# Optimization experiments

Hardware: AMD Instinct MI355X
Metric: run time of the kernel (lower is better)

## Reference

```python
import jax, jax.numpy as jnp
import numpy as np

B, L, C, D = 32, 256, 16, 128
WORD_VOCAB, CHR_VOCAB = 50000, 128


def conv1d(x, w, b):
    # x: [N, D, T], w: [D_out, D_in, 3], torch Conv1d (cross-correlation), padding=1
    y = jax.lax.conv_general_dilated(x, w, window_strides=(1,), padding=[(1, 1)],
                                     dimension_numbers=('NCH', 'OIH', 'NCH'))
    return y + b[None, :, None]


def setup_inputs() -> dict:
    key = jax.random.key(0)
    k1, k2, k3, k4, k5, k6, k7, k8 = jax.random.split(key, 8)
    word_vector = jax.random.randint(k1, (B, L), 0, WORD_VOCAB)
    words_in_char = jax.random.randint(k2, (B, L, C), 0, CHR_VOCAB)
    # embedding tables, padding_idx=0 -> row 0 is zeros
    word_table = (jax.random.normal(k3, (WORD_VOCAB, D), jnp.float32) * 0.02).at[0].set(0.0)
    chr_table = (jax.random.normal(k4, (CHR_VOCAB, D), jnp.float32) * 0.02).at[0].set(0.0)
    scale = 1.0 / np.sqrt(D * 3)
    conv_chr_w = jax.random.normal(k5, (D, D, 3), jnp.float32) * scale
    conv_chr_b = jax.random.normal(k6, (D,), jnp.float32) * scale
    conv_word_w = jax.random.normal(k7, (D, D, 3), jnp.float32) * scale
    conv_word_b = jax.random.normal(k8, (D,), jnp.float32) * scale
    return dict(word_vector=word_vector, words_in_char=words_in_char,
                word_table=word_table, chr_table=chr_table,
                conv_chr_w=conv_chr_w, conv_chr_b=conv_chr_b,
                conv_word_w=conv_word_w, conv_word_b=conv_word_b)


def reference(word_vector, words_in_char, word_table, chr_table,
              conv_chr_w, conv_chr_b, conv_word_w, conv_word_b):
    # --- char path (batched version of the per-word Python loop) ---
    chr_emb = chr_table[words_in_char]                       # [B, L, C, D]
    x = chr_emb.reshape(B * L, C, D).transpose(0, 2, 1)      # [B*L, D, C]
    word_conv = conv1d(x, conv_chr_w, conv_chr_b)            # [B*L, D, C]
    char_feats = word_conv.max(axis=2).reshape(B, L, D)      # max over char positions
    # --- word path ---
    word_emb = word_table[word_vector]                       # [B, L, D]
    out = conv1d(word_emb.transpose(0, 2, 1), conv_word_w, conv_word_b)  # [B, D, L]
    # stack both branch outputs into one array: [2, B, D, L]
    return jnp.stack([out, char_feats.transpose(0, 2, 1)])
```

## Files before the change

kernel.cpp:

```cpp
#include <hip/hip_runtime.h>

typedef __attribute__((ext_vector_type(8))) short short8;
typedef __attribute__((ext_vector_type(2))) float float2_t;
typedef __attribute__((ext_vector_type(4))) float float4_t;
typedef __attribute__((ext_vector_type(16))) float float16_t;

#define NB 32
#define NL 256
#define ND 128
#define OUT_PLANE (NB * ND * NL)
#define XS 136
#define BUFSZ (18 * XS)
#define FR_WORD 49152
#define CHRB 98304

__device__ inline unsigned short f2bf(float f) {
    union { float f; unsigned int i; } c;
    c.f = f;
    unsigned int r = c.i + 0x7FFFu + ((c.i >> 16) & 1u);
    return (unsigned short)(r >> 16);
}

__global__ void make_frags(const float* __restrict__ Wc,
                           const float* __restrict__ Ww,
                           const float* __restrict__ chrT,
                           unsigned short* __restrict__ out) {
    int i = blockIdx.x * 256 + threadIdx.x;
    if (i < FR_WORD) {
        int j    = i & 7;
        int lane = (i >> 3) & 63;
        int nt   = (i >> 9) & 3;
        int s    = i >> 11;
        int dout = nt * 32 + (lane & 31);
        int kk   = s * 16 + ((lane >> 5) & 1) * 8 + j;
        int t    = kk >> 7;
        int d    = kk & 127;
        out[i] = f2bf(Wc[(dout * 128 + d) * 3 + t]);
    } else if (i < CHRB) {
        int ii = i - FR_WORD;
        int j    = ii & 7;
        int lane = (ii >> 3) & 63;
        int nt   = (ii >> 9) & 7;
        int s    = ii >> 12;
        int dout = nt * 16 + (lane & 15);
        int t    = s >> 2;
        int k    = (s & 3) * 32 + ((lane >> 4) & 3) * 8 + j;
        out[i] = f2bf(Ww[(dout * 128 + k) * 3 + t]);
    } else {
        int j = i - CHRB;
        out[i] = f2bf(chrT[j]);
    }
}

__global__ __launch_bounds__(128, 2) void conv_kernel(
    const int* __restrict__ wv, const int* __restrict__ wic,
    const float* __restrict__ wordT,
    const unsigned short* __restrict__ ws,
    const float* __restrict__ biasC, const float* __restrict__ biasW,
    float* __restrict__ out) {
    __shared__ unsigned short X[4][BUFSZ];
    const int tid  = threadIdx.x;
    const int wave = tid >> 6, lane = tid & 63;
    const int bid = blockIdx.x;

    if (bid >= 512) {
        const unsigned short* chrB = ws + CHRB;
        const int w0 = (bid - 512) * 8;
        const int b = w0 >> 8, l0 = w0 & 255;
        const int n32 = lane & 31;
        const int h   = (lane >> 5) & 1;
        const int r15 = lane & 15;
        const int wsel = (lane >> 4) & 1;

        short8 bfrag[24][2];
#pragma unroll
        for (int s = 0; s < 24; ++s)
#pragma unroll
            for (int p = 0; p < 2; ++p)
                bfrag[s][p] = *(const short8*)(
                    ws + (((s * 4 + wave * 2 + p) * 64 + lane) << 3));

        for (int p = tid; p < XS; p += 128)
#pragma unroll
            for (int q = 0; q < 4; ++q) { X[q][p] = 0; X[q][17 * XS + p] = 0; }

        const int ra = tid >> 4, sub = tid & 15;

#pragma unroll
        for (int q = 0; q < 2; ++q) {
            int j0 = wic[(w0 + q) * 16 + ra];
            int j1 = wic[(w0 + q) * 16 + ra + 8];
            short8 g0 = *(const short8*)(chrB + j0 * 128 + sub * 8);
            short8 g1 = *(const short8*)(chrB + j1 * 128 + sub * 8);
            *(short8*)&X[q][(ra + 1) * XS + sub * 8] = g0;
            *(short8*)&X[q][(ra + 9) * XS + sub * 8] = g1;
        }
        int iA0 = wic[(w0 + 2) * 16 + ra];
        int iA1 = wic[(w0 + 2) * 16 + ra + 8];
        int iC0 = wic[(w0 + 3) * 16 + ra];
        int iC1 = wic[(w0 + 3) * 16 + ra + 8];
        __syncthreads();

#pragma unroll
        for (int j = 0; j < 8; j += 2) {
            const unsigned short* abuf = X[(j + wsel) & 3];

            short8 g0, g1;
            if (j < 6) {
                g0 = *(const short8*)(chrB + iA0 * 128 + sub * 8);
                g1 = *(const short8*)(chrB + iA1 * 128 + sub * 8);
            }

            float16_t acc[2];
#pragma unroll
            for (int p = 0; p < 2; ++p)
#pragma unroll
                for (int e = 0; e < 16; ++e) acc[p][e] = 0.f;

#pragma unroll
            for (int s = 0; s < 12; ++s) {
                short8 a = *(const short8*)&abuf[(r15 + (s >> 3)) * XS +
                                                 (s & 7) * 16 + h * 8];
#pragma unroll
                for (int p = 0; p < 2; ++p)
                    acc[p] = __builtin_amdgcn_mfma_f32_32x32x16_bf16(
                        a, bfrag[s][p], acc[p], 0, 0, 0);
            }

            short8 h0, h1;
            if (j < 6) {
                *(short8*)&X[(j + 2) & 3][(ra + 1) * XS + sub * 8] = g0;
                *(short8*)&X[(j + 2) & 3][(ra + 9) * XS + sub * 8] = g1;
                h0 = *(const short8*)(chrB + iC0 * 128 + sub * 8);
                h1 = *(const short8*)(chrB + iC1 * 128 + sub * 8);
                if (j < 4) {
                    iA0 = wic[(w0 + j + 4) * 16 + ra];
                    iA1 = wic[(w0 + j + 4) * 16 + ra + 8];
                    iC0 = wic[(w0 + j + 5) * 16 + ra];
                    iC1 = wic[(w0 + j + 5) * 16 + ra + 8];
                }
            }

#pragma unroll
            for (int s = 12; s < 24; ++s) {
                short8 a = *(const short8*)&abuf[(r15 + (s >> 3)) * XS +
                                                 (s & 7) * 16 + h * 8];
#pragma unroll
                for (int p = 0; p < 2; ++p)
                    acc[p] = __builtin_amdgcn_mfma_f32_32x32x16_bf16(
                        a, bfrag[s][p], acc[p], 0, 0, 0);
            }

            if (j < 6) {
                *(short8*)&X[(j + 3) & 3][(ra + 1) * XS + sub * 8] = h0;
                *(short8*)&X[(j + 3) & 3][(ra + 9) * XS + sub * 8] = h1;
            }

#pragma unroll
            for (int p = 0; p < 2; ++p) {
                float v0 = acc[p][0], v1 = acc[p][8];
#pragma unroll
                for (int e = 1; e < 8; ++e) {
                    v0 = fmaxf(v0, acc[p][e]);
                    v1 = fmaxf(v1, acc[p][e + 8]);
                }
                v0 = fmaxf(v0, __shfl_xor(v0, 32, 64));
                v1 = fmaxf(v1, __shfl_xor(v1, 32, 64));
                int dout = wave * 64 + p * 32 + n32;
                if (lane < 32) {
                    float bc = biasC[dout];
                    float2_t st = {v0 + bc, v1 + bc};
                    *(float2_t*)&out[OUT_PLANE + b * (ND * NL) + dout * NL +
                                     l0 + j] = st;
                }
            }
            __syncthreads();
        }
    } else {
        const int m = lane & 15, quad = lane >> 4;
        const int b = bid >> 4, l0 = (bid & 15) << 4;
        short8 bfrag[12][4];
#pragma unroll
        for (int s = 0; s < 12; ++s)
#pragma unroll
            for (int p = 0; p < 4; ++p)
                bfrag[s][p] = *(const short8*)(
                    ws + FR_WORD + (((s * 8 + wave * 4 + p) * 64 + lane) << 3));
        float bb[4];
#pragma unroll
        for (int p = 0; p < 4; ++p) bb[p] = biasW[wave * 64 + p * 16 + m];

#pragma unroll
        for (int i0 = 0; i0 < 2; ++i0) {
            int i = tid + i0 * 128;
            if (i < 144) {
                int rr = i >> 3, sg = i & 7;
                int l = l0 + rr - 1;
                int idx = (l >= 0 && l < NL) ? wv[b * NL + l] : 0;
                const float4_t* src =
                    (const float4_t*)(wordT + idx * 128 + sg * 16);
                float4_t f0 = src[0], f1 = src[1], f2 = src[2], f3 = src[3];
                unsigned short t16[16];
                t16[0]=f2bf(f0.x); t16[1]=f2bf(f0.y); t16[2]=f2bf(f0.z); t16[3]=f2bf(f0.w);
                t16[4]=f2bf(f1.x); t16[5]=f2bf(f1.y); t16[6]=f2bf(f1.z); t16[7]=f2bf(f1.w);
                t16[8]=f2bf(f2.x); t16[9]=f2bf(f2.y); t16[10]=f2bf(f2.z); t16[11]=f2bf(f2.w);
                t16[12]=f2bf(f3.x); t16[13]=f2bf(f3.y); t16[14]=f2bf(f3.z); t16[15]=f2bf(f3.w);
                *(short8*)&X[0][rr * XS + sg * 16]     = *(const short8*)&t16[0];
                *(short8*)&X[0][rr * XS + sg * 16 + 8] = *(const short8*)&t16[8];
            }
        }
        __syncthreads();

        float4_t acc[4];
#pragma unroll
        for (int p = 0; p < 4; ++p) acc[p] = (float4_t){0.f, 0.f, 0.f, 0.f};
#pragma unroll
        for (int s = 0; s < 12; ++s) {
            short8 a = *(const short8*)&X[0][(m + (s >> 2)) * XS +
                                            (s & 3) * 32 + quad * 8];
#pragma unroll
            for (int p = 0; p < 4; ++p)
                acc[p] = __builtin_amdgcn_mfma_f32_16x16x32_bf16(
                    a, bfrag[s][p], acc[p], 0, 0, 0);
        }

        float* obase = out + b * (ND * NL) + l0 + quad * 4;
#pragma unroll
        for (int p = 0; p < 4; ++p) {
            int dout = wave * 64 + p * 16 + m;
            float4_t pk;
            pk.x = acc[p].x + bb[p];
            pk.y = acc[p].y + bb[p];
            pk.z = acc[p].z + bb[p];
            pk.w = acc[p].w + bb[p];
            *(float4_t*)&obase[dout * NL] = pk;
        }
    }
}

extern "C" void kernel_launch(void* const* d_in, const int* in_sizes, int n_in,
                              void* d_out, int out_size, void* d_ws,
                              size_t ws_size, hipStream_t stream) {
    const int* word_vector   = (const int*)d_in[0];
    const int* words_in_char = (const int*)d_in[1];
    const float* word_table  = (const float*)d_in[2];
    const float* chr_table   = (const float*)d_in[3];
    const float* conv_chr_w  = (const float*)d_in[4];
    const float* conv_chr_b  = (const float*)d_in[5];
    const float* conv_word_w = (const float*)d_in[6];
    const float* conv_word_b = (const float*)d_in[7];
    float* out            = (float*)d_out;
    unsigned short* wsp   = (unsigned short*)d_ws;

    make_frags<<<448, 256, 0, stream>>>(conv_chr_w, conv_word_w, chr_table, wsp);
    conv_kernel<<<1536, 128, 0, stream>>>(word_vector, words_in_char,
                                          word_table, wsp,
                                          conv_chr_b, conv_word_b, out);
}
```

Before: 105.4 us.

## Fuse fragment prep into conv kernel with grid-wide atomic barrier

Merges the bf16 weight/table conversion kernel into the main conv kernel. Each block converts a slice of the workspace, then all blocks wait on a global atomic counter before continuing. The grid shrinks from 1536 to 1024 blocks: every block does a char-path tile, and the first 512 also do a word-path tile. This drops one kernel launch and the gap between launches, but adds a hipMemsetAsync and a spin barrier. The barrier relies on all 1024 blocks being resident at once and can deadlock if they are not.

```diff
diff --git a/kernel.cpp b/kernel.cpp
--- a/kernel.cpp
+++ b/kernel.cpp
@@ -13,6 +13,9 @@
 #define BUFSZ (18 * XS)
 #define FR_WORD 49152
 #define CHRB 98304
+#define WS_ELEMS 114688
+#define FLAG_BYTE_OFF (WS_ELEMS * 2)
+#define GRID 1024
 
 __device__ inline unsigned short f2bf(float f) {
     union { float f; unsigned int i; } c;
@@ -21,51 +24,63 @@
     return (unsigned short)(r >> 16);
 }
 
-__global__ void make_frags(const float* __restrict__ Wc,
-                           const float* __restrict__ Ww,
-                           const float* __restrict__ chrT,
-                           unsigned short* __restrict__ out) {
-    int i = blockIdx.x * 256 + threadIdx.x;
-    if (i < FR_WORD) {
-        int j    = i & 7;
-        int lane = (i >> 3) & 63;
-        int nt   = (i >> 9) & 3;
-        int s    = i >> 11;
-        int dout = nt * 32 + (lane & 31);
-        int kk   = s * 16 + ((lane >> 5) & 1) * 8 + j;
-        int t    = kk >> 7;
-        int d    = kk & 127;
-        out[i] = f2bf(Wc[(dout * 128 + d) * 3 + t]);
-    } else if (i < CHRB) {
-        int ii = i - FR_WORD;
-        int j    = ii & 7;
-        int lane = (ii >> 3) & 63;
-        int nt   = (ii >> 9) & 7;
-        int s    = ii >> 12;
-        int dout = nt * 16 + (lane & 15);
-        int t    = s >> 2;
-        int k    = (s & 3) * 32 + ((lane >> 4) & 3) * 8 + j;
-        out[i] = f2bf(Ww[(dout * 128 + k) * 3 + t]);
-    } else {
-        int j = i - CHRB;
-        out[i] = f2bf(chrT[j]);
-    }
-}
-
-__global__ __launch_bounds__(128, 2) void conv_kernel(
+__global__ __launch_bounds__(128, 2) void conv_all(
     const int* __restrict__ wv, const int* __restrict__ wic,
-    const float* __restrict__ wordT,
-    const unsigned short* __restrict__ ws,
+    const float* __restrict__ wordT, const float* __restrict__ chrT,
+    const float* __restrict__ Wc, const float* __restrict__ Ww,
     const float* __restrict__ biasC, const float* __restrict__ biasW,
+    unsigned short* __restrict__ wsp, unsigned int* __restrict__ flag,
     float* __restrict__ out) {
     __shared__ unsigned short X[4][BUFSZ];
     const int tid  = threadIdx.x;
     const int wave = tid >> 6, lane = tid & 63;
     const int bid = blockIdx.x;
 
-    if (bid >= 512) {
-        const unsigned short* chrB = ws + CHRB;
-        const int w0 = (bid - 512) * 8;
+    if (tid < 112) {
+        int i = bid * 112 + tid;
+        unsigned short val;
+        if (i < FR_WORD) {
+            int j    = i & 7;
+            int ln   = (i >> 3) & 63;
+            int nt   = (i >> 9) & 3;
+            int s    = i >> 11;
+            int dout = nt * 32 + (ln & 31);
+            int kk   = s * 16 + ((ln >> 5) & 1) * 8 + j;
+            int t    = kk >> 7;
+            int d    = kk & 127;
+            val = f2bf(Wc[(dout * 128 + d) * 3 + t]);
+        } else if (i < CHRB) {
+            int ii = i - FR_WORD;
+            int j    = ii & 7;
+            int ln   = (ii >> 3) & 63;
+            int nt   = (ii >> 9) & 7;
+            int s    = ii >> 12;
+            int dout = nt * 16 + (ln & 15);
+            int t    = s >> 2;
+            int k    = (s & 3) * 32 + ((ln >> 4) & 3) * 8 + j;
+            val = f2bf(Ww[(dout * 128 + k) * 3 + t]);
+        } else {
+            val = f2bf(chrT[i - CHRB]);
+        }
+        wsp[i] = val;
+    }
+    for (int p = tid; p < XS; p += 128)
+#pragma unroll
+        for (int q = 0; q < 4; ++q) { X[q][p] = 0; X[q][17 * XS + p] = 0; }
+
+    __threadfence();
+    __syncthreads();
+    if (tid == 0) {
+        atomicAdd(flag, 1u);
+        while (*(volatile unsigned int*)flag < (unsigned int)GRID)
+            __builtin_amdgcn_s_sleep(8);
+    }
+    __syncthreads();
+    __threadfence();
+
+    {
+        const unsigned short* chrB = wsp + CHRB;
+        const int w0 = bid * 8;
         const int b = w0 >> 8, l0 = w0 & 255;
         const int n32 = lane & 31;
         const int h   = (lane >> 5) & 1;
@@ -78,11 +93,7 @@
 #pragma unroll
             for (int p = 0; p < 2; ++p)
                 bfrag[s][p] = *(const short8*)(
-                    ws + (((s * 4 + wave * 2 + p) * 64 + lane) << 3));
-
-        for (int p = tid; p < XS; p += 128)
-#pragma unroll
-            for (int q = 0; q < 4; ++q) { X[q][p] = 0; X[q][17 * XS + p] = 0; }
+                    wsp + (((s * 4 + wave * 2 + p) * 64 + lane) << 3));
 
         const int ra = tid >> 4, sub = tid & 15;
 
@@ -176,7 +187,9 @@
             }
             __syncthreads();
         }
-    } else {
+    }
+
+    if (bid < 512) {
         const int m = lane & 15, quad = lane >> 4;
         const int b = bid >> 4, l0 = (bid & 15) << 4;
         short8 bfrag[12][4];
@@ -185,7 +198,7 @@
 #pragma unroll
             for (int p = 0; p < 4; ++p)
                 bfrag[s][p] = *(const short8*)(
-                    ws + FR_WORD + (((s * 8 + wave * 4 + p) * 64 + lane) << 3));
+                    wsp + FR_WORD + (((s * 8 + wave * 4 + p) * 64 + lane) << 3));
         float bb[4];
 #pragma unroll
         for (int p = 0; p < 4; ++p) bb[p] = biasW[wave * 64 + p * 16 + m];
@@ -251,9 +264,12 @@
     const float* conv_word_b = (const float*)d_in[7];
     float* out            = (float*)d_out;
     unsigned short* wsp   = (unsigned short*)d_ws;
-
-    make_frags<<<448, 256, 0, stream>>>(conv_chr_w, conv_word_w, chr_table, wsp);
-    conv_kernel<<<1536, 128, 0, stream>>>(word_vector, words_in_char,
-                                          word_table, wsp,
-                                          conv_chr_b, conv_word_b, out);
+    unsigned int* flag    = (unsigned int*)((char*)d_ws + FLAG_BYTE_OFF);
+
+    hipMemsetAsync(flag, 0, 4, stream);
+    conv_all<<<GRID, 128, 0, stream>>>(word_vector, words_in_char,
+                                       word_table, chr_table,
+                                       conv_chr_w, conv_word_w,
+                                       conv_chr_b, conv_word_b,
+                                       wsp, flag, out);
 }
```

Result: slower. 243.1 us (+130.7%).
